# Optimization experiments

Measured on AMD Instinct MI355X. Metric: run time of the kernel, lower is better.

Reference implementation:

```python
import jax, jax.numpy as jnp
import numpy as np

HID_X = 64
MLP_RATIO = 4
EPS_NORM = 1e-12  # F.normalize default eps
EPS_RMS = 1e-6


def _l2norm_dim2(w):
    # normalize along dim=-2 (the input-feature axis of each per-sample matrix)
    n = jnp.sqrt(jnp.sum(w * w, axis=-2, keepdims=True))
    return w / jnp.maximum(n, EPS_NORM)


def setup_inputs() -> dict:
    key = jax.random.key(0)
    k1, k2, k3, k4 = jax.random.split(key, 4)
    B, N, D, S = 64, 4096, HID_X, 1024
    total = 3 * D * D * MLP_RATIO
    x = jax.random.normal(k1, (B, N, D), dtype=jnp.float32)
    s = jax.random.normal(k2, (B, S), dtype=jnp.float32)
    W_pg = jax.random.normal(k3, (S, total), dtype=jnp.float32) * 0.02
    b_pg = jax.random.normal(k4, (total,), dtype=jnp.float32) * 0.01
    scale = jnp.ones((D,), dtype=jnp.float32)
    return {"x": x, "s": s, "W_pg": W_pg, "b_pg": b_pg, "scale": scale}


def reference(x, s, W_pg, b_pg, scale):
    B, N, D = x.shape
    H = D * MLP_RATIO
    # hypernetwork: generate per-sample MLP weights
    mlp_params = s @ W_pg + b_pg  # [B, 3*D*H]
    g_p, v_p, f_p = jnp.split(mlp_params, 3, axis=-1)
    fc1_gate = _l2norm_dim2(g_p.reshape(B, D, H))
    fc1_value = _l2norm_dim2(v_p.reshape(B, D, H))
    fc2 = _l2norm_dim2(f_p.reshape(B, H, D))
    # RMSNorm (eps=1e-6)
    rrms = jax.lax.rsqrt(jnp.mean(x * x, axis=-1, keepdims=True) + EPS_RMS)
    xn = x * rrms * scale
    gate = jnp.einsum('bnd,bdh->bnh', xn, fc1_gate)
    value = jnp.einsum('bnd,bdh->bnh', xn, fc1_value)
    h = jax.nn.silu(gate) * value
    out = jnp.einsum('bnh,bhd->bnd', h, fc2) + x
    return out
```

## Files before the change

### kernel.cpp

```cpp
#include <hip/hip_runtime.h>
#include <hip/hip_bf16.h>

#define BB 64
#define NN 4096
#define DD 64
#define HH 256
#define SS 1024
#define TOTAL 49152
#define MAT_ELEMS 16384
#define PSLICE 3145728

typedef __bf16 bf16x8 __attribute__((ext_vector_type(8)));
typedef float  f32x4  __attribute__((ext_vector_type(4)));

__global__ __launch_bounds__(256, 3) void k1_gemm(
    const float* __restrict__ s, const float* __restrict__ W,
    float* __restrict__ partials)
{
    const int nb = blockIdx.x >> 2;
    const int ks = blockIdx.x & 3;
    const int n0 = nb * 256;
    const int k0 = ks * 256;
    const int t  = threadIdx.x;
    const int tx = t & 31;
    const int ty = t >> 5;

    __shared__ float sB[32 * 256];
    __shared__ float sAT[32 * 68];

    float acc[8][8] = {};

    const int brow = t >> 3;
    const int bcol = (t & 7) * 4;
    const float* wp = &W[(size_t)(k0 + brow) * TOTAL + n0 + bcol];
    const int am  = t >> 2;
    const int akq = (t & 3) * 8;
    const float* ap = &s[(size_t)am * SS + k0 + akq];

    float4 pB[8];
    #pragma unroll
    for (int jj = 0; jj < 8; jj++) pB[jj] = *(const float4*)(wp + jj * 32);
    float4 pA0 = *(const float4*)(ap);
    float4 pA1 = *(const float4*)(ap + 4);

    for (int st = 0; st < 8; st++) {
        #pragma unroll
        for (int jj = 0; jj < 8; jj++)
            *(float4*)&sB[brow * 256 + bcol + jj * 32] = pB[jj];
        sAT[(akq + 0) * 68 + am] = pA0.x;
        sAT[(akq + 1) * 68 + am] = pA0.y;
        sAT[(akq + 2) * 68 + am] = pA0.z;
        sAT[(akq + 3) * 68 + am] = pA0.w;
        sAT[(akq + 4) * 68 + am] = pA1.x;
        sAT[(akq + 5) * 68 + am] = pA1.y;
        sAT[(akq + 6) * 68 + am] = pA1.z;
        sAT[(akq + 7) * 68 + am] = pA1.w;
        __syncthreads();
        if (st < 7) {
            const float* wpn = wp + (size_t)(st + 1) * 32 * TOTAL;
            #pragma unroll
            for (int jj = 0; jj < 8; jj++) pB[jj] = *(const float4*)(wpn + jj * 32);
            pA0 = *(const float4*)(ap + (st + 1) * 32);
            pA1 = *(const float4*)(ap + (st + 1) * 32 + 4);
        }
        #pragma unroll 8
        for (int kk = 0; kk < 32; kk++) {
            float4 b0 = *(const float4*)&sB[kk * 256 + tx * 8];
            float4 b1 = *(const float4*)&sB[kk * 256 + tx * 8 + 4];
            float4 a0 = *(const float4*)&sAT[kk * 68 + ty * 8];
            float4 a1 = *(const float4*)&sAT[kk * 68 + ty * 8 + 4];
            float av[8] = {a0.x, a0.y, a0.z, a0.w, a1.x, a1.y, a1.z, a1.w};
            float bv[8] = {b0.x, b0.y, b0.z, b0.w, b1.x, b1.y, b1.z, b1.w};
            #pragma unroll
            for (int r = 0; r < 8; r++)
                #pragma unroll
                for (int c = 0; c < 8; c++)
                    acc[r][c] += av[r] * bv[c];
        }
        __syncthreads();
    }

    float* pp = partials + (size_t)ks * PSLICE;
    #pragma unroll
    for (int r = 0; r < 8; r++) {
        int m = ty * 8 + r;
        float* o = pp + (size_t)m * TOTAL + n0 + tx * 8;
        float4 o0 = {acc[r][0], acc[r][1], acc[r][2], acc[r][3]};
        float4 o1 = {acc[r][4], acc[r][5], acc[r][6], acc[r][7]};
        *(float4*)(o)     = o0;
        *(float4*)(o + 4) = o1;
    }
}

__global__ __launch_bounds__(256) void k2_fc1(
    const float* __restrict__ partials, const float* __restrict__ bias,
    __bf16* __restrict__ WgT, __bf16* __restrict__ WvT)
{
    const int b    = blockIdx.x >> 4;
    const int mat  = (blockIdx.x >> 3) & 1;
    const int hg   = blockIdx.x & 7;
    const int t    = threadIdx.x;
    const int hh   = t & 31;
    const int dseg = t >> 5;
    const int h    = hg * 32 + hh;

    __shared__ float psum[8 * 32];
    __shared__ float rnorm[32];

    const size_t base = (size_t)b * TOTAL + mat * MAT_ELEMS;
    const float* p0 = partials + base;
    const float* p1 = p0 + PSLICE;
    const float* p2 = p1 + PSLICE;
    const float* p3 = p2 + PSLICE;
    const float* bi = bias + mat * MAT_ELEMS;

    float val[8];
    float ss = 0.f;
    #pragma unroll
    for (int j = 0; j < 8; j++) {
        int off = (dseg * 8 + j) * 256 + h;
        float v = p0[off] + p1[off] + p2[off] + p3[off] + bi[off];
        val[j] = v;
        ss += v * v;
    }
    psum[dseg * 32 + hh] = ss;
    __syncthreads();
    if (t < 32) {
        float s2 = 0.f;
        #pragma unroll
        for (int g = 0; g < 8; g++) s2 += psum[g * 32 + t];
        rnorm[t] = 1.0f / fmaxf(sqrtf(s2), 1e-12f);
    }
    __syncthreads();
    float rn = rnorm[hh];
    __bf16* dst = (mat ? WvT : WgT) + (size_t)b * MAT_ELEMS + (size_t)h * 64 + dseg * 8;
    bf16x8 ov;
    #pragma unroll
    for (int j = 0; j < 8; j++) ov[j] = (__bf16)(val[j] * rn);
    *(bf16x8*)dst = ov;
}

__global__ __launch_bounds__(256) void k2_fc2(
    const float* __restrict__ partials, const float* __restrict__ bias,
    __bf16* __restrict__ WfT)
{
    const int b    = blockIdx.x >> 3;
    const int dg   = blockIdx.x & 7;
    const int t    = threadIdx.x;
    const int dd   = t & 7;
    const int hseg = t >> 3;

    __shared__ float psum[32 * 8];
    __shared__ float rnorm[8];

    const size_t base = (size_t)b * TOTAL + 2 * MAT_ELEMS;
    const float* p0 = partials + base;
    const float* p1 = p0 + PSLICE;
    const float* p2 = p1 + PSLICE;
    const float* p3 = p2 + PSLICE;
    const float* bi = bias + 2 * MAT_ELEMS;

    float val[8];
    float ss = 0.f;
    #pragma unroll
    for (int j = 0; j < 8; j++) {
        int off = (hseg * 8 + j) * 64 + dg * 8 + dd;
        float v = p0[off] + p1[off] + p2[off] + p3[off] + bi[off];
        val[j] = v;
        ss += v * v;
    }
    psum[hseg * 8 + dd] = ss;
    __syncthreads();
    if (t < 8) {
        float s2 = 0.f;
        #pragma unroll
        for (int g = 0; g < 32; g++) s2 += psum[g * 8 + t];
        rnorm[t] = 1.0f / fmaxf(sqrtf(s2), 1e-12f);
    }
    __syncthreads();
    float rn = rnorm[dd];
    __bf16* dst = WfT + (size_t)b * MAT_ELEMS + (size_t)(dg * 8 + dd) * 256 + hseg * 8;
    bf16x8 ov;
    #pragma unroll
    for (int j = 0; j < 8; j++) ov[j] = (__bf16)(val[j] * rn);
    *(bf16x8*)dst = ov;
}

__global__ __launch_bounds__(256, 4) void k3_fused(
    const float* __restrict__ x, const float* __restrict__ scale,
    const __bf16* __restrict__ WgT, const __bf16* __restrict__ WvT,
    const __bf16* __restrict__ WfT, float* __restrict__ out)
{
    const int b    = blockIdx.x >> 5;
    const int rb   = blockIdx.x & 31;
    const int t    = threadIdx.x;
    const int w    = t >> 6;
    const int lane = t & 63;
    const int l15  = lane & 15;
    const int quad = lane >> 4;

    __shared__ __bf16 h_sh[4 * 32 * 136];

    const size_t row_base = ((size_t)b * NN + rb * 128) * DD;

    float sc[16];
    *(float4*)&sc[0]  = *(const float4*)&scale[quad * 8];
    *(float4*)&sc[4]  = *(const float4*)&scale[quad * 8 + 4];
    *(float4*)&sc[8]  = *(const float4*)&scale[32 + quad * 8];
    *(float4*)&sc[12] = *(const float4*)&scale[32 + quad * 8 + 4];

    bf16x8 afrag[2][2];
    #pragma unroll
    for (int mt = 0; mt < 2; mt++) {
        int row = w * 32 + mt * 16 + l15;
        const float* xp = &x[row_base + (size_t)row * DD + quad * 8];
        float v[16];
        *(float4*)&v[0]  = *(const float4*)(xp);
        *(float4*)&v[4]  = *(const float4*)(xp + 4);
        *(float4*)&v[8]  = *(const float4*)(xp + 32);
        *(float4*)&v[12] = *(const float4*)(xp + 36);
        float ss = 0.f;
        #pragma unroll
        for (int j = 0; j < 16; j++) ss += v[j] * v[j];
        ss += __shfl_xor(ss, 16, 64);
        ss += __shfl_xor(ss, 32, 64);
        float rr = rsqrtf(ss * (1.0f / 64.0f) + 1e-6f);
        #pragma unroll
        for (int j = 0; j < 8; j++) {
            afrag[mt][0][j] = (__bf16)(v[j] * rr * sc[j]);
            afrag[mt][1][j] = (__bf16)(v[8 + j] * rr * sc[8 + j]);
        }
    }

    f32x4 oacc[2][4] = {};
    const __bf16* wg_b = WgT + (size_t)b * MAT_ELEMS;
    const __bf16* wv_b = WvT + (size_t)b * MAT_ELEMS;
    const __bf16* wf_b = WfT + (size_t)b * MAT_ELEMS;
    __bf16* hbuf = &h_sh[w * 32 * 136];

    for (int half = 0; half < 2; half++) {
        #pragma unroll
        for (int npl = 0; npl < 4; npl++) {
            const int np = half * 4 + npl;
            bf16x8 bg[2][2], bv[2][2];
            #pragma unroll
            for (int sub = 0; sub < 2; sub++) {
                int nt = np * 2 + sub;
                const __bf16* gp = &wg_b[(nt * 16 + l15) * 64 + quad * 8];
                const __bf16* vp = &wv_b[(nt * 16 + l15) * 64 + quad * 8];
                bg[sub][0] = *(const bf16x8*)(gp);
                bg[sub][1] = *(const bf16x8*)(gp + 32);
                bv[sub][0] = *(const bf16x8*)(vp);
                bv[sub][1] = *(const bf16x8*)(vp + 32);
            }
            #pragma unroll
            for (int sub = 0; sub < 2; sub++) {
                #pragma unroll
                for (int mt = 0; mt < 2; mt++) {
                    f32x4 g = {0.f, 0.f, 0.f, 0.f}, vv = {0.f, 0.f, 0.f, 0.f};
                    g  = __builtin_amdgcn_mfma_f32_16x16x32_bf16(afrag[mt][0], bg[sub][0], g, 0, 0, 0);
                    g  = __builtin_amdgcn_mfma_f32_16x16x32_bf16(afrag[mt][1], bg[sub][1], g, 0, 0, 0);
                    vv = __builtin_amdgcn_mfma_f32_16x16x32_bf16(afrag[mt][0], bv[sub][0], vv, 0, 0, 0);
                    vv = __builtin_amdgcn_mfma_f32_16x16x32_bf16(afrag[mt][1], bv[sub][1], vv, 0, 0, 0);
                    #pragma unroll
                    for (int r = 0; r < 4; r++) {
                        float gv = g[r];
                        float sig = __builtin_amdgcn_rcpf(1.0f + __expf(-gv));
                        float hval = gv * sig * vv[r];
                        hbuf[(mt * 16 + quad * 4 + r) * 136 + npl * 32 + sub * 16 + l15] = (__bf16)hval;
                    }
                }
            }
        }
        #pragma unroll
        for (int kpl = 0; kpl < 4; kpl++) {
            const int kp = half * 4 + kpl;
            bf16x8 bf[4];
            #pragma unroll
            for (int dt = 0; dt < 4; dt++)
                bf[dt] = *(const bf16x8*)&wf_b[(dt * 16 + l15) * 256 + kp * 32 + quad * 8];
            #pragma unroll
            for (int mt = 0; mt < 2; mt++) {
                bf16x8 ah = *(const bf16x8*)&hbuf[(mt * 16 + l15) * 136 + kpl * 32 + quad * 8];
                #pragma unroll
                for (int dt = 0; dt < 4; dt++)
                    oacc[mt][dt] = __builtin_amdgcn_mfma_f32_16x16x32_bf16(ah, bf[dt], oacc[mt][dt], 0, 0, 0);
            }
        }
    }

    #pragma unroll
    for (int mt = 0; mt < 2; mt++) {
        int r0 = w * 32 + mt * 16 + quad * 4;
        #pragma unroll
        for (int rg = 0; rg < 4; rg++) {
            size_t roff = row_base + (size_t)(r0 + rg) * DD;
            #pragma unroll
            for (int dt = 0; dt < 4; dt++) {
                int col = dt * 16 + l15;
                out[roff + col] = oacc[mt][dt][rg] + x[roff + col];
            }
        }
    }
}

extern "C" void kernel_launch(void* const* d_in, const int* in_sizes, int n_in,
                              void* d_out, int out_size, void* d_ws, size_t ws_size,
                              hipStream_t stream)
{
    const float* x     = (const float*)d_in[0];
    const float* s     = (const float*)d_in[1];
    const float* W_pg  = (const float*)d_in[2];
    const float* b_pg  = (const float*)d_in[3];
    const float* scale = (const float*)d_in[4];
    float* out = (float*)d_out;

    char* ws = (char*)d_ws;
    float*  partials = (float*)ws;
    __bf16* WgT      = (__bf16*)(ws + 50331648);
    __bf16* WvT      = (__bf16*)(ws + 52428800);
    __bf16* WfT      = (__bf16*)(ws + 54525952);

    k1_gemm<<<768, 256, 0, stream>>>(s, W_pg, partials);
    k2_fc1<<<BB * 16, 256, 0, stream>>>(partials, b_pg, WgT, WvT);
    k2_fc2<<<BB * 8, 256, 0, stream>>>(partials, b_pg, WfT);
    k3_fused<<<BB * 32, 256, 0, stream>>>(x, scale, WgT, WvT, WfT, out);
}
```

Baseline: 497.8 us.

## Run hypernetwork GEMM on bf16 MFMA with split-bf16 precision and no split-K

```diff
diff --git a/kernel.cpp b/kernel.cpp
--- a/kernel.cpp
+++ b/kernel.cpp
@@ -8,93 +8,103 @@
 #define SS 1024
 #define TOTAL 49152
 #define MAT_ELEMS 16384
-#define PSLICE 3145728
 
 typedef __bf16 bf16x8 __attribute__((ext_vector_type(8)));
 typedef float  f32x4  __attribute__((ext_vector_type(4)));
 
+__global__ __launch_bounds__(256) void k0_sconv(
+    const float* __restrict__ s, __bf16* __restrict__ sHi, __bf16* __restrict__ sLo)
+{
+    const int idx  = blockIdx.x * 256 + threadIdx.x;
+    const int lane = idx & 63;
+    const int fs   = idx >> 6;
+    const int mf   = fs & 3;
+    const int ks   = fs >> 2;
+    const int m = mf * 16 + (lane & 15);
+    const int k = ks * 32 + (lane >> 4) * 8;
+    const float* sp = &s[(size_t)m * SS + k];
+    float4 v0 = *(const float4*)(sp);
+    float4 v1 = *(const float4*)(sp + 4);
+    float vv[8] = {v0.x, v0.y, v0.z, v0.w, v1.x, v1.y, v1.z, v1.w};
+    bf16x8 hi, lo;
+    #pragma unroll
+    for (int j = 0; j < 8; j++) {
+        __bf16 h = (__bf16)vv[j];
+        hi[j] = h;
+        lo[j] = (__bf16)(vv[j] - (float)h);
+    }
+    *(bf16x8*)&sHi[(size_t)idx * 8] = hi;
+    *(bf16x8*)&sLo[(size_t)idx * 8] = lo;
+}
+
 __global__ __launch_bounds__(256, 3) void k1_gemm(
-    const float* __restrict__ s, const float* __restrict__ W,
-    float* __restrict__ partials)
-{
-    const int nb = blockIdx.x >> 2;
-    const int ks = blockIdx.x & 3;
-    const int n0 = nb * 256;
-    const int k0 = ks * 256;
-    const int t  = threadIdx.x;
-    const int tx = t & 31;
-    const int ty = t >> 5;
-
-    __shared__ float sB[32 * 256];
-    __shared__ float sAT[32 * 68];
-
-    float acc[8][8] = {};
-
-    const int brow = t >> 3;
-    const int bcol = (t & 7) * 4;
-    const float* wp = &W[(size_t)(k0 + brow) * TOTAL + n0 + bcol];
-    const int am  = t >> 2;
-    const int akq = (t & 3) * 8;
-    const float* ap = &s[(size_t)am * SS + k0 + akq];
-
-    float4 pB[8];
-    #pragma unroll
-    for (int jj = 0; jj < 8; jj++) pB[jj] = *(const float4*)(wp + jj * 32);
-    float4 pA0 = *(const float4*)(ap);
-    float4 pA1 = *(const float4*)(ap + 4);
-
-    for (int st = 0; st < 8; st++) {
-        #pragma unroll
-        for (int jj = 0; jj < 8; jj++)
-            *(float4*)&sB[brow * 256 + bcol + jj * 32] = pB[jj];
-        sAT[(akq + 0) * 68 + am] = pA0.x;
-        sAT[(akq + 1) * 68 + am] = pA0.y;
-        sAT[(akq + 2) * 68 + am] = pA0.z;
-        sAT[(akq + 3) * 68 + am] = pA0.w;
-        sAT[(akq + 4) * 68 + am] = pA1.x;
-        sAT[(akq + 5) * 68 + am] = pA1.y;
-        sAT[(akq + 6) * 68 + am] = pA1.z;
-        sAT[(akq + 7) * 68 + am] = pA1.w;
+    const __bf16* __restrict__ sHi, const __bf16* __restrict__ sLo,
+    const float* __restrict__ W, const float* __restrict__ bias,
+    float* __restrict__ params)
+{
+    const int n0   = blockIdx.x * 64;
+    const int t    = threadIdx.x;
+    const int w    = t >> 6;
+    const int lane = t & 63;
+    const int l15  = lane & 15;
+    const int quad = lane >> 4;
+    const int wn   = w * 16;
+
+    __shared__ float sW[32 * 66];
+
+    f32x4 acc[4] = {};
+
+    const int srow = t >> 3;
+    const int scol = (t & 7) * 8;
+    const float* wp = &W[(size_t)srow * TOTAL + n0 + scol];
+
+    float4 p0 = *(const float4*)(wp);
+    float4 p1 = *(const float4*)(wp + 4);
+
+    for (int ks = 0; ks < 32; ks++) {
+        *(float4*)&sW[srow * 66 + scol]     = p0;
+        *(float4*)&sW[srow * 66 + scol + 4] = p1;
         __syncthreads();
-        if (st < 7) {
-            const float* wpn = wp + (size_t)(st + 1) * 32 * TOTAL;
-            #pragma unroll
-            for (int jj = 0; jj < 8; jj++) pB[jj] = *(const float4*)(wpn + jj * 32);
-            pA0 = *(const float4*)(ap + (st + 1) * 32);
-            pA1 = *(const float4*)(ap + (st + 1) * 32 + 4);
-        }
-        #pragma unroll 8
-        for (int kk = 0; kk < 32; kk++) {
-            float4 b0 = *(const float4*)&sB[kk * 256 + tx * 8];
-            float4 b1 = *(const float4*)&sB[kk * 256 + tx * 8 + 4];
-            float4 a0 = *(const float4*)&sAT[kk * 68 + ty * 8];
-            float4 a1 = *(const float4*)&sAT[kk * 68 + ty * 8 + 4];
-            float av[8] = {a0.x, a0.y, a0.z, a0.w, a1.x, a1.y, a1.z, a1.w};
-            float bv[8] = {b0.x, b0.y, b0.z, b0.w, b1.x, b1.y, b1.z, b1.w};
-            #pragma unroll
-            for (int r = 0; r < 8; r++)
-                #pragma unroll
-                for (int c = 0; c < 8; c++)
-                    acc[r][c] += av[r] * bv[c];
+        if (ks < 31) {
+            const float* wpn = wp + (size_t)(ks + 1) * 32 * TOTAL;
+            p0 = *(const float4*)(wpn);
+            p1 = *(const float4*)(wpn + 4);
+        }
+        bf16x8 bHi, bLo;
+        #pragma unroll
+        for (int j = 0; j < 8; j++) {
+            float v  = sW[(quad * 8 + j) * 66 + wn + l15];
+            __bf16 h = (__bf16)v;
+            bHi[j] = h;
+            bLo[j] = (__bf16)(v - (float)h);
+        }
+        const __bf16* ah = &sHi[((size_t)(ks * 4) * 64 + lane) * 8];
+        const __bf16* al = &sLo[((size_t)(ks * 4) * 64 + lane) * 8];
+        #pragma unroll
+        for (int mf = 0; mf < 4; mf++) {
+            bf16x8 aHi = *(const bf16x8*)(ah + mf * 512);
+            bf16x8 aLo = *(const bf16x8*)(al + mf * 512);
+            acc[mf] = __builtin_amdgcn_mfma_f32_16x16x32_bf16(aHi, bHi, acc[mf], 0, 0, 0);
+            acc[mf] = __builtin_amdgcn_mfma_f32_16x16x32_bf16(aHi, bLo, acc[mf], 0, 0, 0);
+            acc[mf] = __builtin_amdgcn_mfma_f32_16x16x32_bf16(aLo, bHi, acc[mf], 0, 0, 0);
         }
         __syncthreads();
     }
 
-    float* pp = partials + (size_t)ks * PSLICE;
-    #pragma unroll
-    for (int r = 0; r < 8; r++) {
-        int m = ty * 8 + r;
-        float* o = pp + (size_t)m * TOTAL + n0 + tx * 8;
-        float4 o0 = {acc[r][0], acc[r][1], acc[r][2], acc[r][3]};
-        float4 o1 = {acc[r][4], acc[r][5], acc[r][6], acc[r][7]};
-        *(float4*)(o)     = o0;
-        *(float4*)(o + 4) = o1;
+    const int n = n0 + wn + l15;
+    const float bv = bias[n];
+    #pragma unroll
+    for (int mf = 0; mf < 4; mf++) {
+        #pragma unroll
+        for (int r = 0; r < 4; r++) {
+            int m = mf * 16 + quad * 4 + r;
+            params[(size_t)m * TOTAL + n] = acc[mf][r] + bv;
+        }
     }
 }
 
 __global__ __launch_bounds__(256) void k2_fc1(
-    const float* __restrict__ partials, const float* __restrict__ bias,
-    __bf16* __restrict__ WgT, __bf16* __restrict__ WvT)
+    const float* __restrict__ params, __bf16* __restrict__ WgT, __bf16* __restrict__ WvT)
 {
     const int b    = blockIdx.x >> 4;
     const int mat  = (blockIdx.x >> 3) & 1;
@@ -107,19 +117,14 @@
     __shared__ float psum[8 * 32];
     __shared__ float rnorm[32];
 
-    const size_t base = (size_t)b * TOTAL + mat * MAT_ELEMS;
-    const float* p0 = partials + base;
-    const float* p1 = p0 + PSLICE;
-    const float* p2 = p1 + PSLICE;
-    const float* p3 = p2 + PSLICE;
-    const float* bi = bias + mat * MAT_ELEMS;
+    const float* p0 = params + (size_t)b * TOTAL + mat * MAT_ELEMS;
 
     float val[8];
     float ss = 0.f;
     #pragma unroll
     for (int j = 0; j < 8; j++) {
         int off = (dseg * 8 + j) * 256 + h;
-        float v = p0[off] + p1[off] + p2[off] + p3[off] + bi[off];
+        float v = p0[off];
         val[j] = v;
         ss += v * v;
     }
@@ -141,8 +146,7 @@
 }
 
 __global__ __launch_bounds__(256) void k2_fc2(
-    const float* __restrict__ partials, const float* __restrict__ bias,
-    __bf16* __restrict__ WfT)
+    const float* __restrict__ params, __bf16* __restrict__ WfT)
 {
     const int b    = blockIdx.x >> 3;
     const int dg   = blockIdx.x & 7;
@@ -153,19 +157,14 @@
     __shared__ float psum[32 * 8];
     __shared__ float rnorm[8];
 
-    const size_t base = (size_t)b * TOTAL + 2 * MAT_ELEMS;
-    const float* p0 = partials + base;
-    const float* p1 = p0 + PSLICE;
-    const float* p2 = p1 + PSLICE;
-    const float* p3 = p2 + PSLICE;
-    const float* bi = bias + 2 * MAT_ELEMS;
+    const float* p0 = params + (size_t)b * TOTAL + 2 * MAT_ELEMS;
 
     float val[8];
     float ss = 0.f;
     #pragma unroll
     for (int j = 0; j < 8; j++) {
         int off = (hseg * 8 + j) * 64 + dg * 8 + dd;
-        float v = p0[off] + p1[off] + p2[off] + p3[off] + bi[off];
+        float v = p0[off];
         val[j] = v;
         ss += v * v;
     }
@@ -316,13 +315,16 @@
     float* out = (float*)d_out;
 
     char* ws = (char*)d_ws;
-    float*  partials = (float*)ws;
-    __bf16* WgT      = (__bf16*)(ws + 50331648);
-    __bf16* WvT      = (__bf16*)(ws + 52428800);
-    __bf16* WfT      = (__bf16*)(ws + 54525952);
-
-    k1_gemm<<<768, 256, 0, stream>>>(s, W_pg, partials);
-    k2_fc1<<<BB * 16, 256, 0, stream>>>(partials, b_pg, WgT, WvT);
-    k2_fc2<<<BB * 8, 256, 0, stream>>>(partials, b_pg, WfT);
+    float*  params = (float*)ws;
+    __bf16* WgT    = (__bf16*)(ws + 12582912);
+    __bf16* WvT    = (__bf16*)(ws + 14680064);
+    __bf16* WfT    = (__bf16*)(ws + 16777216);
+    __bf16* sHi    = (__bf16*)(ws + 18874368);
+    __bf16* sLo    = (__bf16*)(ws + 19005440);
+
+    k0_sconv<<<32, 256, 0, stream>>>(s, sHi, sLo);
+    k1_gemm<<<TOTAL / 64, 256, 0, stream>>>(sHi, sLo, W_pg, b_pg, params);
+    k2_fc1<<<BB * 16, 256, 0, stream>>>(params, WgT, WvT);
+    k2_fc2<<<BB * 8, 256, 0, stream>>>(params, WfT);
     k3_fused<<<BB * 32, 256, 0, stream>>>(x, scale, WgT, WvT, WfT, out);
 }
```

Result: faster. 443.5 us (-10.9%).
